# Kernel optimization log

Hardware: AMD Instinct MI355X
Metric: run time of the kernel (lower is better)

## Reference

```python
import jax, jax.numpy as jnp
import numpy as np

H = 128          # hidden_channels
N_USER = 100000
N_ITEM = 50000
E = 1000000      # number of labeled edges


def setup_inputs() -> dict:
    key = jax.random.key(0)
    ks = jax.random.split(key, 6)
    z_user = jax.random.normal(ks[0], (N_USER, H), dtype=jnp.float32)
    z_item = jax.random.normal(ks[1], (N_ITEM, H), dtype=jnp.float32)
    row = jax.random.randint(ks[2], (E,), 0, N_USER, dtype=jnp.int64 if jax.config.jax_enable_x64 else jnp.int32)
    col = jax.random.randint(ks[3], (E,), 0, N_ITEM, dtype=jnp.int64 if jax.config.jax_enable_x64 else jnp.int32)
    W1 = jax.random.normal(ks[4], (2 * H, H), dtype=jnp.float32) / np.sqrt(2 * H)
    b1 = jnp.zeros((H,), dtype=jnp.float32)
    W2 = jax.random.normal(ks[5], (H, 1), dtype=jnp.float32) / np.sqrt(H)
    b2 = jnp.zeros((1,), dtype=jnp.float32)
    return {"z_user": z_user, "z_item": z_item, "row": row, "col": col,
            "W1": W1, "b1": b1, "W2": W2, "b2": b2}


def reference(z_user, z_item, row, col, W1, b1, W2, b2):
    # z = cat([z_user[row], z_item[col]], -1); lin1(z).relu(); lin2 -> view(-1)
    # Split W1 so we never materialize the [E, 2H] concat explicitly as one buffer:
    # cat([a, b]) @ W1 == a @ W1[:H] + b @ W1[H:]
    W1u, W1i = W1[:H], W1[H:]
    h = z_user[row] @ W1u + z_item[col] @ W1i + b1          # [E, H]
    h = jax.nn.relu(h)
    out = h @ W2 + b2                                        # [E, 1]
    return out.reshape(-1)
```

## Files before the change

kernel.cpp:

```cpp
#include <hip/hip_runtime.h>

#define HH 128
#define BU 8
#define BI 32
#define NBKT (BU * BI)
#define SCHUNK 2048
#define GPUC 8192

typedef __attribute__((ext_vector_type(8))) short bf16x8;
typedef __attribute__((ext_vector_type(4))) float f32x4;
typedef _Float16 h2 __attribute__((ext_vector_type(2)));

#if __has_builtin(__builtin_amdgcn_fdot2)
#define FDOT2(a, b, c) __builtin_amdgcn_fdot2((a), (b), (c), false)
#else
#define FDOT2(a, b, c) ((c) + (float)(a)[0] * (float)(b)[0] + (float)(a)[1] * (float)(b)[1])
#endif

__device__ inline unsigned short f2bf(float f) {
    unsigned u = __builtin_bit_cast(unsigned, f);
    u += 0x7FFF + ((u >> 16) & 1);
    return (unsigned short)(u >> 16);
}
__device__ inline unsigned short f2h(float f) {
    return __builtin_bit_cast(unsigned short, (_Float16)f);
}

__global__ __launch_bounds__(256) void prep_kernel(
    const float* __restrict__ W1, unsigned short* __restrict__ Wt,
    const int* __restrict__ row, const int* __restrict__ col,
    unsigned* __restrict__ cursor, unsigned* __restrict__ srt,
    unsigned* __restrict__ invpos, int E, unsigned n_user, unsigned n_item, int cap)
{
    const int t = threadIdx.x;
    if ((int)blockIdx.x < 16) {
        const int gid = blockIdx.x * 256 + t;
        const int h   = gid >> 11;
        const int c   = (gid >> 4) & 127;
        const int kc  = gid & 15;
        const float* src = W1 + (size_t)(h * 128 + kc * 8) * HH + c;
        unsigned short v[8];
        #pragma unroll
        for (int d = 0; d < 8; ++d)
            v[d] = f2bf(src[(size_t)d * HH]);
        uint4 pack;
        pack.x = (unsigned)v[0] | ((unsigned)v[1] << 16);
        pack.y = (unsigned)v[2] | ((unsigned)v[3] << 16);
        pack.z = (unsigned)v[4] | ((unsigned)v[5] << 16);
        pack.w = (unsigned)v[6] | ((unsigned)v[7] << 16);
        *(uint4*)(Wt + (size_t)h * 16384 + c * 128 + ((kc ^ (c & 15)) << 3)) = pack;
        return;
    }
    __shared__ unsigned lh[NBKT];
    __shared__ unsigned gb[NBKT];
    __shared__ unsigned lc[NBKT];
    const int base = ((int)blockIdx.x - 16) * SCHUNK;

    int uu[SCHUNK / 256], ii[SCHUNK / 256];
    lh[t] = 0;
    __syncthreads();
    #pragma unroll
    for (int k = 0; k < SCHUNK / 256; ++k) {
        int e = base + k * 256 + t;
        if (e < E) {
            uu[k] = row[e]; ii[k] = col[e];
            unsigned uc = ((unsigned)uu[k] * BU) / n_user;
            unsigned ic = ((unsigned)ii[k] * BI) / n_item;
            atomicAdd(&lh[uc * BI + ic], 1u);
        }
    }
    __syncthreads();
    gb[t] = lh[t] ? (unsigned)(t * cap) + atomicAdd(&cursor[t], lh[t]) : 0u;
    lc[t] = 0;
    __syncthreads();
    #pragma unroll
    for (int k = 0; k < SCHUNK / 256; ++k) {
        int e = base + k * 256 + t;
        if (e < E) {
            unsigned uc = ((unsigned)uu[k] * BU) / n_user;
            unsigned ic = ((unsigned)ii[k] * BI) / n_item;
            int b = (int)(uc * BI + ic);
            unsigned ucbase = (uc * n_user + 7u) >> 3;
            unsigned r   = atomicAdd(&lc[b], 1u);
            unsigned pos = gb[b] + r;
            srt[pos]  = (((unsigned)uu[k] - ucbase) << 16) | (unsigned)ii[k];
            invpos[e] = pos;
        }
    }
}

__global__ __launch_bounds__(256) void project_kernel(
    const float* __restrict__ Zu, const float* __restrict__ Zi,
    const unsigned short* __restrict__ Wt, const float* __restrict__ b1,
    unsigned short* __restrict__ Pu, unsigned short* __restrict__ Pi,
    int n_user, int n_item, int utiles, int itiles)
{
    __shared__ unsigned short sWt[128 * 128];
    __shared__ unsigned short sOut[64 * 136];

    const int t    = threadIdx.x;
    const int wave = t >> 6;
    const int lane = t & 63;
    const int l16  = lane & 15;
    const int lk8  = (lane >> 4) * 8;
    const int total = utiles + itiles;

    int staged = -1;

    for (int tid = blockIdx.x; tid < total; tid += gridDim.x) {
        const bool isUser = (tid < utiles);
        const int  half   = isUser ? 0 : 1;
        const float* __restrict__ Z = isUser ? Zu : Zi;
        unsigned short* __restrict__ P = isUser ? Pu : Pi;
        const int nrows = isUser ? n_user : n_item;
        const int rbase = (isUser ? tid : (tid - utiles)) << 6;

        if (half != staged) {
            __syncthreads();
            const unsigned short* src = Wt + (size_t)half * 16384;
            #pragma unroll
            for (int i = 0; i < 16; ++i) {
                int off = (i * 256 + t) * 8;
                *(uint4*)(sWt + off) = *(const uint4*)(src + off);
            }
            __syncthreads();
            staged = half;
        }

        float b1r[8];
        #pragma unroll
        for (int nt = 0; nt < 8; ++nt)
            b1r[nt] = isUser ? b1[nt * 16 + l16] : 0.f;

        f32x4 acc[8];
        #pragma unroll
        for (int nt = 0; nt < 8; ++nt) acc[nt] = (f32x4)0.f;

        int m = rbase + wave * 16 + l16;
        if (m > nrows - 1) m = nrows - 1;
        const float* Zrow = Z + (size_t)m * HH;

        #pragma unroll
        for (int kk = 0; kk < 4; ++kk) {
            float4 z0 = *(const float4*)(Zrow + kk * 32 + lk8);
            float4 z1 = *(const float4*)(Zrow + kk * 32 + lk8 + 4);
            bf16x8 a;
            a[0] = (short)f2bf(z0.x); a[1] = (short)f2bf(z0.y);
            a[2] = (short)f2bf(z0.z); a[3] = (short)f2bf(z0.w);
            a[4] = (short)f2bf(z1.x); a[5] = (short)f2bf(z1.y);
            a[6] = (short)f2bf(z1.z); a[7] = (short)f2bf(z1.w);

            const int chunkSw = ((kk * 4 + (lane >> 4)) ^ l16) << 3;
            #pragma unroll
            for (int nt = 0; nt < 8; ++nt) {
                int c = nt * 16 + l16;
                bf16x8 b = *(const bf16x8*)(sWt + c * 128 + chunkSw);
                acc[nt] = __builtin_amdgcn_mfma_f32_16x16x32_bf16(a, b, acc[nt], 0, 0, 0);
            }
        }

        __syncthreads();
        #pragma unroll
        for (int nt = 0; nt < 8; ++nt) {
            int colc = nt * 16 + l16;
            #pragma unroll
            for (int r = 0; r < 4; ++r) {
                int orow = wave * 16 + (lane >> 4) * 4 + r;
                sOut[orow * 136 + colc] = f2h(acc[nt][r] + b1r[nt]);
            }
        }
        __syncthreads();
        #pragma unroll
        for (int i = 0; i < 4; ++i) {
            int idx = t + i * 256;
            int r   = idx >> 4;
            int ch  = idx & 15;
            int grow = rbase + r;
            if (grow < nrows)
                *(uint4*)(P + (size_t)grow * HH + ch * 8) =
                    *(const uint4*)(sOut + r * 136 + ch * 8);
        }
    }
}

__global__ __launch_bounds__(256) void edge_sorted_kernel(
    const unsigned short* __restrict__ Pu, const unsigned short* __restrict__ Pi,
    const unsigned* __restrict__ srt, const unsigned* __restrict__ cursor,
    const float* __restrict__ W2, const float* __restrict__ b2,
    float* __restrict__ psorted, int cap, int n_user)
{
    const int uc     = blockIdx.x & (BU - 1);
    const int jj     = blockIdx.x >> 3;
    const int g      = threadIdx.x >> 3;
    const int lane8  = threadIdx.x & 7;
    const int gg     = jj * 32 + g;
    const int c0     = lane8 * 16;
    const int ucbase = (int)(((unsigned)uc * (unsigned)n_user + 7u) >> 3);

    h2 w2h[8];
    #pragma unroll
    for (int j = 0; j < 8; ++j) {
        w2h[j][0] = (_Float16)W2[c0 + 2 * j];
        w2h[j][1] = (_Float16)W2[c0 + 2 * j + 1];
    }
    const float b2s = b2[0];
    const h2 hz = {(_Float16)0, (_Float16)0};

    #pragma unroll 1
    for (int ic = 0; ic < BI; ++ic) {
        const int b    = uc * BI + ic;
        const int S    = b * cap;
        const int Tend = S + (int)cursor[b];
        for (int p = S + gg; p < Tend; p += GPUC) {
            unsigned pk = srt[p];
            int u  = ucbase + (int)(pk >> 16);
            int it = (int)(pk & 0xFFFFu);
            const unsigned short* pur = Pu + (size_t)u  * HH + c0;
            const unsigned short* pir = Pi + (size_t)it * HH + c0;
            uint4 a0 = *(const uint4*)pur;
            uint4 a1 = *(const uint4*)(pur + 8);
            uint4 c0v = *(const uint4*)pir;
            uint4 c1v = *(const uint4*)(pir + 8);
            unsigned aw[8] = {a0.x, a0.y, a0.z, a0.w, a1.x, a1.y, a1.z, a1.w};
            unsigned cw[8] = {c0v.x, c0v.y, c0v.z, c0v.w, c1v.x, c1v.y, c1v.z, c1v.w};
            float acc = 0.f;
            #pragma unroll
            for (int q = 0; q < 8; ++q) {
                h2 s = __builtin_bit_cast(h2, aw[q]) + __builtin_bit_cast(h2, cw[q]);
                s = __builtin_elementwise_max(s, hz);
                acc = FDOT2(s, w2h[q], acc);
            }
            acc += __shfl_xor(acc, 4, 64);
            acc += __shfl_xor(acc, 2, 64);
            acc += __shfl_xor(acc, 1, 64);
            if (lane8 == 0) psorted[p] = acc + b2s;
        }
    }
}

__global__ __launch_bounds__(256) void permute_kernel(
    const float* __restrict__ psorted, const unsigned* __restrict__ invpos,
    float* __restrict__ out, int E)
{
    int i  = blockIdx.x * blockDim.x + threadIdx.x;
    int st = gridDim.x * blockDim.x;
    for (int e = i; e < E; e += st)
        out[e] = psorted[invpos[e]];
}

__global__ __launch_bounds__(256) void edge_fp16_kernel(
    const unsigned short* __restrict__ Pu, const unsigned short* __restrict__ Pi,
    const int* __restrict__ row, const int* __restrict__ col,
    const float* __restrict__ W2, const float* __restrict__ b2,
    float* __restrict__ out, int E)
{
    const int lane8  = threadIdx.x & 7;
    const int gid    = (blockIdx.x * blockDim.x + threadIdx.x) >> 3;
    const int stride = (gridDim.x * blockDim.x) >> 3;
    const int c0     = lane8 * 16;

    h2 w2h[8];
    #pragma unroll
    for (int j = 0; j < 8; ++j) {
        w2h[j][0] = (_Float16)W2[c0 + 2 * j];
        w2h[j][1] = (_Float16)W2[c0 + 2 * j + 1];
    }
    const float b2s = b2[0];
    const h2 hz = {(_Float16)0, (_Float16)0};

    for (int e = gid; e < E; e += stride) {
        int u = row[e], it = col[e];
        const unsigned short* pur = Pu + (size_t)u  * HH + c0;
        const unsigned short* pir = Pi + (size_t)it * HH + c0;
        uint4 a0 = *(const uint4*)pur;
        uint4 a1 = *(const uint4*)(pur + 8);
        uint4 c0v = *(const uint4*)pir;
        uint4 c1v = *(const uint4*)(pir + 8);
        unsigned aw[8] = {a0.x, a0.y, a0.z, a0.w, a1.x, a1.y, a1.z, a1.w};
        unsigned cw[8] = {c0v.x, c0v.y, c0v.z, c0v.w, c1v.x, c1v.y, c1v.z, c1v.w};
        float acc = 0.f;
        #pragma unroll
        for (int q = 0; q < 8; ++q) {
            h2 s = __builtin_bit_cast(h2, aw[q]) + __builtin_bit_cast(h2, cw[q]);
            s = __builtin_elementwise_max(s, hz);
            acc = FDOT2(s, w2h[q], acc);
        }
        acc += __shfl_xor(acc, 4, 64);
        acc += __shfl_xor(acc, 2, 64);
        acc += __shfl_xor(acc, 1, 64);
        if (lane8 == 0) out[e] = acc + b2s;
    }
}

__global__ __launch_bounds__(256) void edge_direct_kernel(
    const float* __restrict__ zu, const float* __restrict__ zi,
    const int* __restrict__ row, const int* __restrict__ col,
    const float* __restrict__ W1, const float* __restrict__ b1,
    const float* __restrict__ W2, const float* __restrict__ b2,
    float* __restrict__ out, int E)
{
    const int lane   = threadIdx.x & 31;
    const int gid    = (blockIdx.x * blockDim.x + threadIdx.x) >> 5;
    const int stride = (gridDim.x * blockDim.x) >> 5;
    const int c0     = lane * 4;

    const float4 b1v = *(const float4*)(b1 + c0);
    const float4 w2v = *(const float4*)(W2 + c0);
    const float  b2s = b2[0];

    for (int e = gid; e < E; e += stride) {
        int u  = row[e];
        int it = col[e];
        const float* zur = zu + (size_t)u  * HH;
        const float* zir = zi + (size_t)it * HH;
        float4 acc = b1v;
        for (int k = 0; k < HH; ++k) {
            float  zk = zur[k];
            float4 w  = *(const float4*)(W1 + (size_t)k * HH + c0);
            acc.x = fmaf(zk, w.x, acc.x);
            acc.y = fmaf(zk, w.y, acc.y);
            acc.z = fmaf(zk, w.z, acc.z);
            acc.w = fmaf(zk, w.w, acc.w);
        }
        for (int k = 0; k < HH; ++k) {
            float  zk = zir[k];
            float4 w  = *(const float4*)(W1 + (size_t)(HH + k) * HH + c0);
            acc.x = fmaf(zk, w.x, acc.x);
            acc.y = fmaf(zk, w.y, acc.y);
            acc.z = fmaf(zk, w.z, acc.z);
            acc.w = fmaf(zk, w.w, acc.w);
        }
        float p = fmaxf(acc.x, 0.f) * w2v.x;
        p = fmaf(fmaxf(acc.y, 0.f), w2v.y, p);
        p = fmaf(fmaxf(acc.z, 0.f), w2v.z, p);
        p = fmaf(fmaxf(acc.w, 0.f), w2v.w, p);
        #pragma unroll
        for (int m = 16; m >= 1; m >>= 1)
            p += __shfl_xor(p, m, 64);
        if (lane == 0) out[e] = p + b2s;
    }
}

static inline size_t align256(size_t x) { return (x + 255) & ~(size_t)255; }

extern "C" void kernel_launch(void* const* d_in, const int* in_sizes, int n_in,
                              void* d_out, int out_size, void* d_ws, size_t ws_size,
                              hipStream_t stream)
{
    const float* z_user = (const float*)d_in[0];
    const float* z_item = (const float*)d_in[1];
    const int*   row    = (const int*)d_in[2];
    const int*   col    = (const int*)d_in[3];
    const float* W1     = (const float*)d_in[4];
    const float* b1     = (const float*)d_in[5];
    const float* W2     = (const float*)d_in[6];
    const float* b2     = (const float*)d_in[7];
    float*       out    = (float*)d_out;

    const int n_user = in_sizes[0] / HH;
    const int n_item = in_sizes[1] / HH;
    const int E      = in_sizes[2];

    const int capBase = (E + NBKT - 1) / NBKT;
    const int cap     = capBase + capBase / 4 + 64;
    const size_t padded = (size_t)cap * NBKT;

    const size_t offWt  = 0;
    const size_t offPu  = align256(offWt  + 32768 * 2);
    const size_t offPi  = align256(offPu  + (size_t)n_user * HH * 2);
    const size_t offSrt = align256(offPi  + (size_t)n_item * HH * 2);
    const size_t offPs  = align256(offSrt + padded * 4);
    const size_t offInv = align256(offPs  + padded * 4);
    const size_t offCur = align256(offInv + (size_t)E * 4);
    const size_t needSort = align256(offCur + NBKT * 4);
    const size_t needProj = align256(offPi + (size_t)n_item * HH * 2);

    const bool sortable = (n_user >= BU) && (n_item >= BI) &&
                          (n_item < 65536) && (n_user / BU + 1 < 65536) &&
                          (n_user <= (1 << 17)) && (ws_size >= needSort);

    const int utiles = (n_user + 63) >> 6;
    const int itiles = (n_item + 63) >> 6;
    const int total  = utiles + itiles;
    const int pgrid  = total < 768 ? total : 768;
    const int scatBlocks = (E + SCHUNK - 1) / SCHUNK;

    if (sortable) {
        unsigned short* Wt  = (unsigned short*)((char*)d_ws + offWt);
        unsigned short* Pu  = (unsigned short*)((char*)d_ws + offPu);
        unsigned short* Pi  = (unsigned short*)((char*)d_ws + offPi);
        unsigned*       srt = (unsigned*)((char*)d_ws + offSrt);
        float*          ps  = (float*)((char*)d_ws + offPs);
        unsigned*       inv = (unsigned*)((char*)d_ws + offInv);
        unsigned*       cur = (unsigned*)((char*)d_ws + offCur);

        hipMemsetAsync(cur, 0, NBKT * 4, stream);
        prep_kernel<<<16 + scatBlocks, 256, 0, stream>>>(
            W1, Wt, row, col, cur, srt, inv, E, (unsigned)n_user, (unsigned)n_item, cap);
        project_kernel<<<pgrid, 256, 0, stream>>>(
            z_user, z_item, Wt, b1, Pu, Pi, n_user, n_item, utiles, itiles);
        edge_sorted_kernel<<<2048, 256, 0, stream>>>(Pu, Pi, srt, cur, W2, b2, ps, cap, n_user);
        permute_kernel<<<1024, 256, 0, stream>>>(ps, inv, out, E);
    } else if (ws_size >= needProj) {
        unsigned short* Wt = (unsigned short*)((char*)d_ws + offWt);
        unsigned short* Pu = (unsigned short*)((char*)d_ws + offPu);
        unsigned short* Pi = (unsigned short*)((char*)d_ws + offPi);
        prep_kernel<<<16, 256, 0, stream>>>(
            W1, Wt, row, col, (unsigned*)nullptr, (unsigned*)nullptr, (unsigned*)nullptr,
            0, (unsigned)n_user, (unsigned)n_item, cap);
        project_kernel<<<pgrid, 256, 0, stream>>>(
            z_user, z_item, Wt, b1, Pu, Pi, n_user, n_item, utiles, itiles);
        edge_fp16_kernel<<<2048, 256, 0, stream>>>(Pu, Pi, row, col, W2, b2, out, E);
    } else {
        edge_direct_kernel<<<2048, 256, 0, stream>>>(z_user, z_item, row, col, W1, b1, W2, b2, out, E);
    }
}
```

Baseline: 97.60 us.

## Process two edges per lane group, use nontemporal streams, enlarge sort chunk

The per-edge gather loop now handles two sorted edges per 8-lane group per iteration, issuing both edges' gathers together to raise memory-level parallelism. Streaming arrays (srt, invpos, psorted, out) are read and written with nontemporal hints so they do not displace the projected embedding rows from cache. The sort chunk size is doubled so each block bins twice as many edges. In exchange, register pressure goes up, and the B-edge bounds handling adds a predicate on every iteration.

```diff
diff --git a/kernel.cpp b/kernel.cpp
--- a/kernel.cpp
+++ b/kernel.cpp
@@ -4,7 +4,7 @@
 #define BU 8
 #define BI 32
 #define NBKT (BU * BI)
-#define SCHUNK 2048
+#define SCHUNK 4096
 #define GPUC 8192
 
 typedef __attribute__((ext_vector_type(8))) short bf16x8;
@@ -83,8 +83,9 @@
             unsigned ucbase = (uc * n_user + 7u) >> 3;
             unsigned r   = atomicAdd(&lc[b], 1u);
             unsigned pos = gb[b] + r;
-            srt[pos]  = (((unsigned)uu[k] - ucbase) << 16) | (unsigned)ii[k];
-            invpos[e] = pos;
+            __builtin_nontemporal_store(
+                (((unsigned)uu[k] - ucbase) << 16) | (unsigned)ii[k], srt + pos);
+            __builtin_nontemporal_store(pos, invpos + e);
         }
     }
 }
@@ -211,29 +212,48 @@
         const int b    = uc * BI + ic;
         const int S    = b * cap;
         const int Tend = S + (int)cursor[b];
-        for (int p = S + gg; p < Tend; p += GPUC) {
-            unsigned pk = srt[p];
-            int u  = ucbase + (int)(pk >> 16);
-            int it = (int)(pk & 0xFFFFu);
-            const unsigned short* pur = Pu + (size_t)u  * HH + c0;
-            const unsigned short* pir = Pi + (size_t)it * HH + c0;
-            uint4 a0 = *(const uint4*)pur;
-            uint4 a1 = *(const uint4*)(pur + 8);
-            uint4 c0v = *(const uint4*)pir;
-            uint4 c1v = *(const uint4*)(pir + 8);
-            unsigned aw[8] = {a0.x, a0.y, a0.z, a0.w, a1.x, a1.y, a1.z, a1.w};
-            unsigned cw[8] = {c0v.x, c0v.y, c0v.z, c0v.w, c1v.x, c1v.y, c1v.z, c1v.w};
-            float acc = 0.f;
+        #pragma unroll 1
+        for (int p0 = S + 2 * gg; p0 < Tend; p0 += 2 * GPUC) {
+            const bool hasB = (p0 + 1 < Tend);
+            unsigned pkA = __builtin_nontemporal_load(srt + p0);
+            unsigned pkB = hasB ? __builtin_nontemporal_load(srt + p0 + 1) : pkA;
+            int uA = ucbase + (int)(pkA >> 16), iA = (int)(pkA & 0xFFFFu);
+            int uB = ucbase + (int)(pkB >> 16), iB = (int)(pkB & 0xFFFFu);
+            const unsigned short* puA = Pu + (size_t)uA * HH + c0;
+            const unsigned short* piA = Pi + (size_t)iA * HH + c0;
+            const unsigned short* puB = Pu + (size_t)uB * HH + c0;
+            const unsigned short* piB = Pi + (size_t)iB * HH + c0;
+            uint4 a0 = *(const uint4*)puA;
+            uint4 a1 = *(const uint4*)(puA + 8);
+            uint4 c0v = *(const uint4*)piA;
+            uint4 c1v = *(const uint4*)(piA + 8);
+            uint4 e0 = *(const uint4*)puB;
+            uint4 e1 = *(const uint4*)(puB + 8);
+            uint4 f0 = *(const uint4*)piB;
+            uint4 f1 = *(const uint4*)(piB + 8);
+            unsigned awA[8] = {a0.x, a0.y, a0.z, a0.w, a1.x, a1.y, a1.z, a1.w};
+            unsigned cwA[8] = {c0v.x, c0v.y, c0v.z, c0v.w, c1v.x, c1v.y, c1v.z, c1v.w};
+            unsigned awB[8] = {e0.x, e0.y, e0.z, e0.w, e1.x, e1.y, e1.z, e1.w};
+            unsigned cwB[8] = {f0.x, f0.y, f0.z, f0.w, f1.x, f1.y, f1.z, f1.w};
+            float accA = 0.f, accB = 0.f;
             #pragma unroll
             for (int q = 0; q < 8; ++q) {
-                h2 s = __builtin_bit_cast(h2, aw[q]) + __builtin_bit_cast(h2, cw[q]);
-                s = __builtin_elementwise_max(s, hz);
-                acc = FDOT2(s, w2h[q], acc);
-            }
-            acc += __shfl_xor(acc, 4, 64);
-            acc += __shfl_xor(acc, 2, 64);
-            acc += __shfl_xor(acc, 1, 64);
-            if (lane8 == 0) psorted[p] = acc + b2s;
+                h2 sA = __builtin_bit_cast(h2, awA[q]) + __builtin_bit_cast(h2, cwA[q]);
+                h2 sB = __builtin_bit_cast(h2, awB[q]) + __builtin_bit_cast(h2, cwB[q]);
+                sA = __builtin_elementwise_max(sA, hz);
+                sB = __builtin_elementwise_max(sB, hz);
+                accA = FDOT2(sA, w2h[q], accA);
+                accB = FDOT2(sB, w2h[q], accB);
+            }
+            #pragma unroll
+            for (int m = 4; m >= 1; m >>= 1) {
+                accA += __shfl_xor(accA, m, 64);
+                accB += __shfl_xor(accB, m, 64);
+            }
+            if (lane8 == 0) {
+                __builtin_nontemporal_store(accA + b2s, psorted + p0);
+                if (hasB) __builtin_nontemporal_store(accB + b2s, psorted + p0 + 1);
+            }
         }
     }
 }
@@ -244,8 +264,10 @@
 {
     int i  = blockIdx.x * blockDim.x + threadIdx.x;
     int st = gridDim.x * blockDim.x;
-    for (int e = i; e < E; e += st)
-        out[e] = psorted[invpos[e]];
+    for (int e = i; e < E; e += st) {
+        unsigned ip = __builtin_nontemporal_load(invpos + e);
+        __builtin_nontemporal_store(psorted[ip], out + e);
+    }
 }
 
 __global__ __launch_bounds__(256) void edge_fp16_kernel(
```

Result: slower. 133.1 us (+36.4%).
